# Kernel tuning notes

Hardware: AMD Instinct MI355X
Metric: run time of the kernel (lower is better)

Reference implementation:

```python
import jax, jax.numpy as jnp
import numpy as np

N = 100000          # nodes
E = 3200000         # edges (avg degree 32)
F_IN = 128
HID = [128, 256, 128, 64, 32]
EPS = 1e-5


def setup_inputs() -> dict:
    key = jax.random.key(0)
    ks = jax.random.split(key, 64)
    inp = {}
    inp["x"] = jax.random.normal(ks[0], (N, F_IN), dtype=jnp.float32)
    inp["edge_index"] = jax.random.randint(ks[1], (2, E), 0, N, dtype=jnp.int64)
    dims = [F_IN] + HID
    k = 2
    for i in range(len(HID)):
        fan_in = dims[i]
        inp[f"W{i}"] = jax.random.normal(ks[k], (dims[i], dims[i + 1]), dtype=jnp.float32) / np.sqrt(fan_in); k += 1
        inp[f"b{i}"] = jnp.zeros((dims[i + 1],), dtype=jnp.float32)
        inp[f"g{i}"] = jnp.ones((dims[i + 1],), dtype=jnp.float32)
        inp[f"be{i}"] = jnp.zeros((dims[i + 1],), dtype=jnp.float32)
    inp["fc_w"] = jax.random.normal(ks[k], (HID[-1], 1), dtype=jnp.float32) / np.sqrt(HID[-1])
    inp["fc_b"] = jnp.zeros((1,), dtype=jnp.float32)
    return inp


def _gcn_forward(x, edge_index, Ws, bs, gs, bes, fc_w, fc_b):
    src, dst = edge_index[0], edge_index[1]
    # symmetric-normalized adjacency with self-loops (PyG GCNConv default,
    # edge_weight=None -> all-ones). deg = in-degree + 1 (self-loop).
    deg = jax.ops.segment_sum(jnp.ones((E,), x.dtype), dst, num_segments=N) + 1.0
    dis = jax.lax.rsqrt(deg)                 # deg^{-1/2}
    di = 1.0 / deg                           # self-loop norm deg^{-1}
    norm = (dis[src] * dis[dst])[:, None]    # [E,1]
    for W, b, g, be in zip(Ws, bs, gs, bes):
        h = x @ W                                                        # [N,d']
        x = jax.ops.segment_sum(norm * h[src], dst, num_segments=N)
        x = x + di[:, None] * h + b                                      # conv out
        mu = jnp.mean(x, axis=0)
        var = jnp.mean(jnp.square(x - mu), axis=0)
        x = (x - mu) * jax.lax.rsqrt(var + EPS) * g + be                 # BatchNorm1d
        x = jax.nn.relu(x)                                               # dropout = eval identity
    edge_emb = x[src] * x[dst]                                           # [E, 32]
    return jax.nn.sigmoid(edge_emb @ fc_w + fc_b)                        # [E, 1]


def reference(x, edge_index, W0, b0, g0, be0, W1, b1, g1, be1, W2, b2, g2, be2,
              W3, b3, g3, be3, W4, b4, g4, be4, fc_w, fc_b):
    Ws = [W0, W1, W2, W3, W4]
    bs = [b0, b1, b2, b3, b4]
    gs = [g0, g1, g2, g3, g4]
    bes = [be0, be1, be2, be3, be4]
    return _gcn_forward(x, edge_index, Ws, bs, gs, bes, fc_w, fc_b)
```

## Files before the change

kernel.cpp:

```cpp
#include <hip/hip_runtime.h>
#include <hip/hip_fp16.h>
#include <cstddef>

#define NN 100000
#define EE 3200000
#define EPSB 1e-5f
#define NB 391
#define BCAP 10240
#define BNBLK 512

typedef _Float16 half8 __attribute__((ext_vector_type(8)));
typedef float floatx4 __attribute__((ext_vector_type(4)));


__global__ __launch_bounds__(256) void k_bscat(const int* __restrict__ src,
                                               const int* __restrict__ dst,
                                               int* __restrict__ bcur,
                                               unsigned* __restrict__ barr) {
    __shared__ int hist[NB];
    __shared__ int base[NB];
    int tid = threadIdx.x;
    for (int b = tid; b < NB; b += 256) hist[b] = 0;
    __syncthreads();
    int e0 = blockIdx.x * 4096;
    int d[16], s[16];
    #pragma unroll
    for (int j = 0; j < 16; j++) {
        int e = e0 + j * 256 + tid;
        if (e < EE) {
            d[j] = dst[e];
            s[j] = src[e];
            atomicAdd(&hist[d[j] >> 8], 1);
        } else d[j] = -1;
    }
    __syncthreads();
    for (int b = tid; b < NB; b += 256) {
        int c = hist[b];
        base[b] = (c > 0) ? atomicAdd(&bcur[b], c) : 0;
        hist[b] = 0;
    }
    __syncthreads();
    #pragma unroll
    for (int j = 0; j < 16; j++) {
        if (d[j] >= 0) {
            int b = d[j] >> 8;
            int r = atomicAdd(&hist[b], 1);
            barr[(size_t)b * BCAP + base[b] + r] =
                (unsigned)s[j] | ((unsigned)(d[j] & 255) << 17);
        }
    }
}

__global__ __launch_bounds__(1024) void k_bdeg(const int* __restrict__ bcur,
                                               const unsigned* __restrict__ barr,
                                               int* __restrict__ degcnt,
                                               float* __restrict__ dis) {
    __shared__ int h[256];
    int b = blockIdx.x;
    if (threadIdx.x < 256) h[threadIdx.x] = 0;
    __syncthreads();
    int cnt = bcur[b];
    const unsigned* p = barr + (size_t)b * BCAP;
    for (int t = threadIdx.x; t < cnt; t += 1024)
        atomicAdd(&h[(p[t] >> 17) & 255], 1);
    __syncthreads();
    if (threadIdx.x < 256) {
        int node = (b << 8) + threadIdx.x;
        if (node < NN) {
            int dg = h[threadIdx.x];
            degcnt[node] = dg;
            dis[node] = rsqrtf((float)dg + 1.0f);
        }
    }
}

__global__ __launch_bounds__(1024) void k_place(const int* __restrict__ bcur,
                                                const unsigned* __restrict__ barr,
                                                const int* __restrict__ rowptr,
                                                int* __restrict__ col) {
    __shared__ int cur[256];
    int b = blockIdx.x;
    if (threadIdx.x < 256) {
        int node = (b << 8) + threadIdx.x;
        cur[threadIdx.x] = (node < NN) ? rowptr[node] : 0;
    }
    __syncthreads();
    int cnt = bcur[b];
    const unsigned* p = barr + (size_t)b * BCAP;
    for (int t = threadIdx.x; t < cnt; t += 1024) {
        unsigned e = p[t];
        int pos = atomicAdd(&cur[(e >> 17) & 255], 1);
        col[pos] = (int)(e & 0x1FFFFu);
    }
}

__global__ void k_scan_block(const int* __restrict__ in, int* __restrict__ out,
                             int* __restrict__ blksum, int n) {
    __shared__ int s[1024];
    int i = blockIdx.x * 1024 + threadIdx.x;
    int v = (i < n) ? in[i] : 0;
    s[threadIdx.x] = v;
    __syncthreads();
    for (int off = 1; off < 1024; off <<= 1) {
        int t = (threadIdx.x >= off) ? s[threadIdx.x - off] : 0;
        __syncthreads();
        s[threadIdx.x] += t;
        __syncthreads();
    }
    if (i < n) out[i] = s[threadIdx.x] - v;
    if (threadIdx.x == 1023) blksum[blockIdx.x] = s[1023];
}

__global__ void k_scan_top(int* __restrict__ blksum, int nb) {
    if (threadIdx.x == 0) {
        int acc = 0;
        for (int b = 0; b < nb; b++) { int v = blksum[b]; blksum[b] = acc; acc += v; }
    }
}

__global__ void k_scan_add(int* __restrict__ out, const int* __restrict__ blksum, int n) {
    int i = blockIdx.x * 1024 + threadIdx.x;
    if (i < n) out[i] += blksum[blockIdx.x];
}


__global__ void k_f2h(const float4* __restrict__ in, uint2* __restrict__ out, int n4) {
    int t = blockIdx.x * blockDim.x + threadIdx.x;
    if (t >= n4) return;
    float4 v = in[t];
    union { __half2 h; unsigned u; } a, b;
    a.h = __floats2half2_rn(v.x, v.y);
    b.h = __floats2half2_rn(v.z, v.w);
    out[t] = make_uint2(a.u, b.u);
}

__global__ void k_wpack_all(const float* __restrict__ W0, const float* __restrict__ W1,
                            const float* __restrict__ W2, const float* __restrict__ W3,
                            const float* __restrict__ W4, __half* __restrict__ Wp) {
    const int offs[6] = {0, 16384, 49152, 81920, 90112, 92160};
    const int Ks[5] = {128, 128, 256, 128, 64};
    const int Ns[5] = {128, 256, 128, 64, 32};
    const float* Ws[5] = {W0, W1, W2, W3, W4};
    int t = blockIdx.x * blockDim.x + threadIdx.x;
    if (t >= 92160) return;
    int l = 0;
    while (t >= offs[l + 1]) l++;
    int local = t - offs[l];
    int N = Ns[l], K = Ks[l];
    int k = local / N, n = local - k * N;
    Wp[(size_t)offs[l] + (size_t)n * K + k] = __float2half(Ws[l][local]);
}


template<int NT, bool OUT16, bool ABN>
__global__ __launch_bounds__(256) void k_mgemm(const void* __restrict__ Av,
                                               const __half* __restrict__ Wp,
                                               void* __restrict__ Cv,
                                               int M, int K, int N,
                                               const float* __restrict__ dis,
                                               const float* __restrict__ bias,
                                               const float* __restrict__ AB) {
    constexpr int TN = NT * 16;
    __shared__ __half Ash[128][40];
    __shared__ __half Bsh[TN][40];
    int tid  = threadIdx.x;
    int wave = tid >> 6;
    int lane = tid & 63;
    int quad = lane >> 4;
    int l16  = lane & 15;
    int bm = blockIdx.x * 128;
    int bn = blockIdx.y * TN;

    floatx4 acc[2][NT];
    #pragma unroll
    for (int mt = 0; mt < 2; mt++)
        #pragma unroll
        for (int nt = 0; nt < NT; nt++)
            acc[mt][nt] = (floatx4){0.f, 0.f, 0.f, 0.f};

    for (int k0 = 0; k0 < K; k0 += 32) {
        #pragma unroll
        for (int it = 0; it < 2; it++) {
            int u = tid + it * 256;
            int row = u >> 2, seg = u & 3;
            int grow = bm + row;
            if (ABN) {
                const float* Af = (const float*)Av;
                int f0 = k0 + seg * 8;
                uint4 o = make_uint4(0, 0, 0, 0);
                if (grow < M) {
                    float4 x0 = *(const float4*)&Af[(size_t)grow * K + f0];
                    float4 x1 = *(const float4*)&Af[(size_t)grow * K + f0 + 4];
                    float4 a0 = *(const float4*)&AB[f0];
                    float4 a1 = *(const float4*)&AB[f0 + 4];
                    float4 c0 = *(const float4*)&AB[K + f0];
                    float4 c1 = *(const float4*)&AB[K + f0 + 4];
                    float h0 = fmaxf(x0.x * a0.x + c0.x, 0.f);
                    float h1 = fmaxf(x0.y * a0.y + c0.y, 0.f);
                    float h2 = fmaxf(x0.z * a0.z + c0.z, 0.f);
                    float h3 = fmaxf(x0.w * a0.w + c0.w, 0.f);
                    float h4 = fmaxf(x1.x * a1.x + c1.x, 0.f);
                    float h5 = fmaxf(x1.y * a1.y + c1.y, 0.f);
                    float h6 = fmaxf(x1.z * a1.z + c1.z, 0.f);
                    float h7 = fmaxf(x1.w * a1.w + c1.w, 0.f);
                    union { __half2 h; unsigned u; } p0, p1, p2, p3;
                    p0.h = __floats2half2_rn(h0, h1);
                    p1.h = __floats2half2_rn(h2, h3);
                    p2.h = __floats2half2_rn(h4, h5);
                    p3.h = __floats2half2_rn(h6, h7);
                    o = make_uint4(p0.u, p1.u, p2.u, p3.u);
                }
                *(uint4*)&Ash[row][seg * 8] = o;
            } else {
                const __half* A = (const __half*)Av;
                uint4 v = make_uint4(0, 0, 0, 0);
                if (grow < M) v = *(const uint4*)&A[(size_t)grow * K + k0 + seg * 8];
                *(uint4*)&Ash[row][seg * 8] = v;
            }
        }
        if (tid < TN * 4) {
            int n = tid >> 2, seg = tid & 3;
            uint4 v = *(const uint4*)&Wp[(size_t)(bn + n) * K + k0 + seg * 8];
            *(uint4*)&Bsh[n][seg * 8] = v;
        }
        __syncthreads();
        half8 a[2], b[NT];
        #pragma unroll
        for (int mt = 0; mt < 2; mt++)
            a[mt] = *(const half8*)&Ash[wave * 32 + mt * 16 + l16][quad * 8];
        #pragma unroll
        for (int nt = 0; nt < NT; nt++)
            b[nt] = *(const half8*)&Bsh[nt * 16 + l16][quad * 8];
        #pragma unroll
        for (int mt = 0; mt < 2; mt++)
            #pragma unroll
            for (int nt = 0; nt < NT; nt++)
                acc[mt][nt] = __builtin_amdgcn_mfma_f32_16x16x32_f16(
                    a[mt], b[nt], acc[mt][nt], 0, 0, 0);
        __syncthreads();
    }

    #pragma unroll
    for (int mt = 0; mt < 2; mt++) {
        #pragma unroll
        for (int r = 0; r < 4; r++) {
            int grow = bm + wave * 32 + mt * 16 + quad * 4 + r;
            if (grow >= M) continue;
            if (OUT16) {
                float ds = dis[grow];
                __half* C = (__half*)Cv;
                #pragma unroll
                for (int nt = 0; nt < NT; nt++) {
                    int gcol = bn + nt * 16 + l16;
                    C[(size_t)grow * N + gcol] = __float2half(ds * acc[mt][nt][r]);
                }
            } else {
                float* C = (float*)Cv;
                #pragma unroll
                for (int nt = 0; nt < NT; nt++) {
                    int gcol = bn + nt * 16 + l16;
                    C[(size_t)grow * N + gcol] = acc[mt][nt][r] + bias[gcol];
                }
            }
        }
    }
}


__global__ __launch_bounds__(256) void k_q8p8(const uint4* __restrict__ H,
                                              uint2* __restrict__ q8,
                                              float* __restrict__ scq, int total) {
    int t = blockIdx.x * 256 + threadIdx.x;
    if (t >= total) return;
    uint4 v = H[t];
    const __half2* hp = (const __half2*)&v;
    float h[8];
    #pragma unroll
    for (int k = 0; k < 4; k++) {
        float2 f = __half22float2(hp[k]);
        h[2 * k] = f.x; h[2 * k + 1] = f.y;
    }
    float m = fabsf(h[0]);
    #pragma unroll
    for (int k = 1; k < 8; k++) m = fmaxf(m, fabsf(h[k]));
    float inv = m > 0.f ? 127.f / m : 0.f;
    unsigned b[8];
    #pragma unroll
    for (int k = 0; k < 8; k++) {
        float f = fminf(fmaxf(h[k] * inv, -127.f), 127.f);
        b[k] = (unsigned)(f + 128.5f);
    }
    q8[t] = make_uint2(b[0] | (b[1] << 8) | (b[2] << 16) | (b[3] << 24),
                       b[4] | (b[5] << 8) | (b[6] << 16) | (b[7] << 24));
    scq[t] = m * (1.f / 127.f);
}

__global__ void k_nscale_q8(const float* __restrict__ X, const float* __restrict__ AB,
                            const float* __restrict__ dis, uint2* __restrict__ q8,
                            float* __restrict__ scq) {
    int t = blockIdx.x * blockDim.x + threadIdx.x;
    if (t >= NN * 16) return;
    int row = t >> 4;
    int f0 = (t & 15) * 8;
    float ds = dis[row];
    float4 x0 = *(const float4*)&X[(size_t)row * 128 + f0];
    float4 x1 = *(const float4*)&X[(size_t)row * 128 + f0 + 4];
    float4 a0 = *(const float4*)&AB[f0];
    float4 a1 = *(const float4*)&AB[f0 + 4];
    float4 c0 = *(const float4*)&AB[128 + f0];
    float4 c1 = *(const float4*)&AB[128 + f0 + 4];
    float h[8];
    h[0] = ds * fmaxf(x0.x * a0.x + c0.x, 0.f);
    h[1] = ds * fmaxf(x0.y * a0.y + c0.y, 0.f);
    h[2] = ds * fmaxf(x0.z * a0.z + c0.z, 0.f);
    h[3] = ds * fmaxf(x0.w * a0.w + c0.w, 0.f);
    h[4] = ds * fmaxf(x1.x * a1.x + c1.x, 0.f);
    h[5] = ds * fmaxf(x1.y * a1.y + c1.y, 0.f);
    h[6] = ds * fmaxf(x1.z * a1.z + c1.z, 0.f);
    h[7] = ds * fmaxf(x1.w * a1.w + c1.w, 0.f);
    float m = h[0];
    #pragma unroll
    for (int k = 1; k < 8; k++) m = fmaxf(m, h[k]);
    m = fmaxf(m, __shfl_xor(m, 1));
    float inv = m > 0.f ? 255.f / m : 0.f;
    unsigned b[8];
    #pragma unroll
    for (int k = 0; k < 8; k++)
        b[k] = (unsigned)(fminf(h[k] * inv, 255.f) + 0.5f);
    q8[t] = make_uint2(b[0] | (b[1] << 8) | (b[2] << 16) | (b[3] << 24),
                       b[4] | (b[5] << 8) | (b[6] << 16) | (b[7] << 24));
    if ((t & 1) == 0) scq[t >> 1] = m * (1.f / 255.f);
}


__device__ __forceinline__ void acc_q8s2(float* acc, const uint4& r,
                                         const float2& s, float& c0, float& c1) {
    const unsigned* w = (const unsigned*)&r;
    c0 += s.x; c1 += s.y;
    #pragma unroll
    for (int q = 0; q < 4; q++) {
        unsigned v = w[q];
        float sq = (q < 2) ? s.x : s.y;
        acc[4 * q + 0] = fmaf(sq, (float)(v & 0xffu), acc[4 * q + 0]);
        acc[4 * q + 1] = fmaf(sq, (float)((v >> 8) & 0xffu), acc[4 * q + 1]);
        acc[4 * q + 2] = fmaf(sq, (float)((v >> 16) & 0xffu), acc[4 * q + 2]);
        acc[4 * q + 3] = fmaf(sq, (float)(v >> 24), acc[4 * q + 3]);
    }
}

template<int TPN>
__global__ __launch_bounds__(256) void k_agg_q8s(const uint4* __restrict__ Q,
                                                 const float* __restrict__ sc,
                                                 float* __restrict__ outf,
                                                 const int* __restrict__ rowptr,
                                                 const int* __restrict__ degcnt,
                                                 const int* __restrict__ colv,
                                                 const float* __restrict__ dis,
                                                 const float* __restrict__ bias) {
    constexpr int G = 256 / TPN;
    int g    = threadIdx.x / TPN;
    int lane = threadIdx.x % TPN;
    int i = blockIdx.x * G + g;
    if (i >= NN) return;
    int beg = rowptr[i];
    int cnt = degcnt[i];
    const uint4*  base = Q + lane;
    const float2* scb  = (const float2*)sc + lane;
    float acc[16] = {};
    float c0 = 0.f, c1 = 0.f;
    int e = 0;
    for (; e + 8 <= cnt; e += 8) {
        int c[8];
        #pragma unroll
        for (int j = 0; j < 8; j++) c[j] = colv[beg + e + j];
        uint4 r[8];
        float2 s[8];
        #pragma unroll
        for (int j = 0; j < 8; j++) {
            r[j] = base[(size_t)c[j] * TPN];
            s[j] = scb[(size_t)c[j] * TPN];
        }
        #pragma unroll
        for (int j = 0; j < 8; j++) acc_q8s2(acc, r[j], s[j], c0, c1);
    }
    for (; e < cnt; e++) {
        int c = colv[beg + e];
        uint4 r = base[(size_t)c * TPN];
        acc_q8s2(acc, r, scb[(size_t)c * TPN], c0, c1);
    }
    uint4 rs = base[(size_t)i * TPN];
    acc_q8s2(acc, rs, scb[(size_t)i * TPN], c0, c1);
    float ds = dis[i];
    float zp0 = 128.f * c0, zp1 = 128.f * c1;
    float o[16];
    #pragma unroll
    for (int k = 0; k < 16; k++) o[k] = ds * (acc[k] - (k < 8 ? zp0 : zp1));
    float4* out = (float4*)outf;
    const float4* bi = (const float4*)bias;
    size_t ob = (size_t)i * (4 * TPN) + lane * 4;
    #pragma unroll
    for (int j = 0; j < 4; j++) {
        float4 b = bi[lane * 4 + j];
        out[ob + j] = make_float4(o[4 * j] + b.x, o[4 * j + 1] + b.y,
                                  o[4 * j + 2] + b.z, o[4 * j + 3] + b.w);
    }
}

__device__ __forceinline__ void acc_q8u(float* acc, const uint4& r, float s) {
    const unsigned* w = (const unsigned*)&r;
    #pragma unroll
    for (int q = 0; q < 4; q++) {
        unsigned v = w[q];
        acc[4 * q + 0] = fmaf(s, (float)(v & 0xffu), acc[4 * q + 0]);
        acc[4 * q + 1] = fmaf(s, (float)((v >> 8) & 0xffu), acc[4 * q + 1]);
        acc[4 * q + 2] = fmaf(s, (float)((v >> 16) & 0xffu), acc[4 * q + 2]);
        acc[4 * q + 3] = fmaf(s, (float)(v >> 24), acc[4 * q + 3]);
    }
}

template<int TPN>
__global__ __launch_bounds__(256) void k_agg_q8u(const uint4* __restrict__ Q,
                                                 const float* __restrict__ sc,
                                                 __half* __restrict__ out16,
                                                 const int* __restrict__ rowptr,
                                                 const int* __restrict__ degcnt,
                                                 const int* __restrict__ colv,
                                                 const float* __restrict__ dis) {
    constexpr int G = 256 / TPN;
    int g    = threadIdx.x / TPN;
    int lane = threadIdx.x % TPN;
    int i = blockIdx.x * G + g;
    if (i >= NN) return;
    int beg = rowptr[i];
    int cnt = degcnt[i];
    const uint4* base = Q + lane;
    const float* scb  = sc + lane;
    float acc[16] = {};
    int e = 0;
    for (; e + 8 <= cnt; e += 8) {
        int c[8];
        #pragma unroll
        for (int j = 0; j < 8; j++) c[j] = colv[beg + e + j];
        uint4 r[8];
        float s[8];
        #pragma unroll
        for (int j = 0; j < 8; j++) {
            r[j] = base[(size_t)c[j] * TPN];
            s[j] = scb[(size_t)c[j] * TPN];
        }
        #pragma unroll
        for (int j = 0; j < 8; j++) acc_q8u(acc, r[j], s[j]);
    }
    for (; e < cnt; e++) {
        int c = colv[beg + e];
        uint4 r = base[(size_t)c * TPN];
        acc_q8u(acc, r, scb[(size_t)c * TPN]);
    }
    uint4 rs = base[(size_t)i * TPN];
    acc_q8u(acc, rs, scb[(size_t)i * TPN]);
    float ds = dis[i];
    float o[16];
    #pragma unroll
    for (int k = 0; k < 16; k++) o[k] = ds * acc[k];
    uint4 ov0, ov1;
    __half2* p0 = (__half2*)&ov0;
    __half2* p1 = (__half2*)&ov1;
    #pragma unroll
    for (int k = 0; k < 4; k++) {
        p0[k] = __floats2half2_rn(o[2 * k], o[2 * k + 1]);
        p1[k] = __floats2half2_rn(o[8 + 2 * k], o[9 + 2 * k]);
    }
    uint4* out = (uint4*)out16;
    size_t ob = (size_t)i * (2 * TPN) + lane * 2;
    out[ob]     = ov0;
    out[ob + 1] = ov1;
}

__device__ __forceinline__ void acc_row(float* acc, const uint4& r) {
    const __half2* hp = (const __half2*)&r;
    #pragma unroll
    for (int k = 0; k < 4; k++) {
        float2 f2 = __half22float2(hp[k]);
        acc[2 * k]     += f2.x;
        acc[2 * k + 1] += f2.y;
    }
}

template<int TPN, bool OUT16>
__global__ __launch_bounds__(256) void k_agg_h(const uint4* __restrict__ Hs,
                                               void* __restrict__ outv,
                                               const int* __restrict__ rowptr,
                                               const int* __restrict__ degcnt,
                                               const int* __restrict__ colv,
                                               const float* __restrict__ dis,
                                               const float* __restrict__ bias) {
    constexpr int G = 256 / TPN;
    int g    = threadIdx.x / TPN;
    int lane = threadIdx.x % TPN;
    int i = blockIdx.x * G + g;
    if (i >= NN) return;
    int beg = rowptr[i];
    int cnt = degcnt[i];
    const uint4* base = Hs + lane;
    float acc[8] = {};
    int e = 0;
    for (; e + 16 <= cnt; e += 16) {
        int c[16];
        #pragma unroll
        for (int j = 0; j < 16; j++) c[j] = colv[beg + e + j];
        uint4 r[16];
        #pragma unroll
        for (int j = 0; j < 16; j++) r[j] = base[(size_t)c[j] * TPN];
        #pragma unroll
        for (int j = 0; j < 16; j++) acc_row(acc, r[j]);
    }
    for (; e + 4 <= cnt; e += 4) {
        int c[4];
        #pragma unroll
        for (int j = 0; j < 4; j++) c[j] = colv[beg + e + j];
        uint4 r[4];
        #pragma unroll
        for (int j = 0; j < 4; j++) r[j] = base[(size_t)c[j] * TPN];
        #pragma unroll
        for (int j = 0; j < 4; j++) acc_row(acc, r[j]);
    }
    for (; e < cnt; e++) {
        uint4 r = base[(size_t)colv[beg + e] * TPN];
        acc_row(acc, r);
    }
    uint4 rs = base[(size_t)i * TPN];
    acc_row(acc, rs);
    float ds = dis[i];
    float o[8];
    #pragma unroll
    for (int k = 0; k < 8; k++) o[k] = ds * acc[k];
    if (OUT16) {
        uint4 ov;
        __half2* op = (__half2*)&ov;
        #pragma unroll
        for (int k = 0; k < 4; k++) op[k] = __floats2half2_rn(o[2 * k], o[2 * k + 1]);
        ((uint4*)outv)[(size_t)i * TPN + lane] = ov;
    } else {
        float4 b0 = ((const float4*)bias)[lane * 2];
        float4 b1 = ((const float4*)bias)[lane * 2 + 1];
        o[0] += b0.x; o[1] += b0.y; o[2] += b0.z; o[3] += b0.w;
        o[4] += b1.x; o[5] += b1.y; o[6] += b1.z; o[7] += b1.w;
        float4* out = (float4*)outv;
        size_t ob = (size_t)i * (2 * TPN) + lane * 2;
        out[ob]     = make_float4(o[0], o[1], o[2], o[3]);
        out[ob + 1] = make_float4(o[4], o[5], o[6], o[7]);
    }
}


template<int D>
__global__ __launch_bounds__(256) void k_bnpart(const float4* __restrict__ X4,
                                                float* __restrict__ partial) {
    constexpr int Q   = D / 4;
    constexpr int RPI = 256 / Q;
    int tq = threadIdx.x % Q;
    int rg = threadIdx.x / Q;
    int chunk = (NN + BNBLK - 1) / BNBLK;
    int r0 = blockIdx.x * chunk;
    int r1 = r0 + chunk; if (r1 > NN) r1 = NN;
    float4 s  = {0.f, 0.f, 0.f, 0.f};
    float4 s2 = {0.f, 0.f, 0.f, 0.f};
    for (int r = r0 + rg; r < r1; r += RPI) {
        float4 v = X4[(size_t)r * Q + tq];
        s.x += v.x; s.y += v.y; s.z += v.z; s.w += v.w;
        s2.x += v.x * v.x; s2.y += v.y * v.y; s2.z += v.z * v.z; s2.w += v.w * v.w;
    }
    __shared__ float4 ls[256], ls2[256];
    ls[threadIdx.x] = s; ls2[threadIdx.x] = s2;
    __syncthreads();
    if (threadIdx.x < Q) {
        float4 a = ls[threadIdx.x], b = ls2[threadIdx.x];
        #pragma unroll
        for (int g = 1; g < RPI; g++) {
            float4 u = ls[g * Q + threadIdx.x], w = ls2[g * Q + threadIdx.x];
            a.x += u.x; a.y += u.y; a.z += u.z; a.w += u.w;
            b.x += w.x; b.y += w.y; b.z += w.z; b.w += w.w;
        }
        *(float4*)&partial[(size_t)blockIdx.x * 2 * D + threadIdx.x * 4]     = a;
        *(float4*)&partial[(size_t)blockIdx.x * 2 * D + D + threadIdx.x * 4] = b;
    }
}

template<int D>
__global__ __launch_bounds__(1024) void k_bnfin2(const float* __restrict__ partial,
                                                 const float* __restrict__ g,
                                                 const float* __restrict__ be,
                                                 float* __restrict__ AB) {
    constexpr int G = 1024 / D;
    int f  = threadIdx.x % D;
    int gr = threadIdx.x / D;
    float sum = 0.f, sq = 0.f;
    for (int b = gr; b < BNBLK; b += G) {
        sum += partial[(size_t)b * 2 * D + f];
        sq  += partial[(size_t)b * 2 * D + D + f];
    }
    __shared__ float ls[1024], ls2[1024];
    ls[threadIdx.x] = sum; ls2[threadIdx.x] = sq;
    __syncthreads();
    if (threadIdx.x < D) {
        float a = ls[threadIdx.x], b = ls2[threadIdx.x];
        for (int k = 1; k < G; k++) {
            a += ls[k * D + threadIdx.x];
            b += ls2[k * D + threadIdx.x];
        }
        float mu  = a / (float)NN;
        float var = b / (float)NN - mu * mu;
        var = fmaxf(var, 0.f);
        float inv = rsqrtf(var + EPSB);
        float sc = g[threadIdx.x] * inv;
        AB[threadIdx.x]     = sc;
        AB[D + threadIdx.x] = be[threadIdx.x] - mu * sc;
    }
}

__global__ void k_norm16(const float4* __restrict__ X, const float* __restrict__ AB,
                         uint2* __restrict__ Y, int d, int total4) {
    int t = blockIdx.x * blockDim.x + threadIdx.x;
    if (t >= total4) return;
    int f0 = (t * 4) & (d - 1);
    float4 v = X[t];
    float a0 = AB[f0],     a1 = AB[f0 + 1], a2 = AB[f0 + 2], a3 = AB[f0 + 3];
    float c0 = AB[d + f0], c1 = AB[d + f0 + 1], c2 = AB[d + f0 + 2], c3 = AB[d + f0 + 3];
    float o0 = fmaxf(v.x * a0 + c0, 0.f);
    float o1 = fmaxf(v.y * a1 + c1, 0.f);
    float o2 = fmaxf(v.z * a2 + c2, 0.f);
    float o3 = fmaxf(v.w * a3 + c3, 0.f);
    union { __half2 h; unsigned u; } p, q;
    p.h = __floats2half2_rn(o0, o1);
    q.h = __floats2half2_rn(o2, o3);
    Y[t] = make_uint2(p.u, q.u);
}


__global__ __launch_bounds__(256) void k_edge16(const uint4* __restrict__ X,
                                                const int* __restrict__ src,
                                                const int* __restrict__ dst,
                                                const float* __restrict__ fcw,
                                                const float* __restrict__ fcb,
                                                float* __restrict__ out) {
    int lane = threadIdx.x & 3;
    size_t t = (size_t)blockIdx.x * 256 + threadIdx.x;
    int eid = (int)(t >> 2);
    if (eid >= EE) return;
    int s = src[eid], d = dst[eid];
    uint4 av = X[(size_t)s * 4 + lane];
    uint4 bv = X[(size_t)d * 4 + lane];
    const __half2* ap = (const __half2*)&av;
    const __half2* bp2 = (const __half2*)&bv;
    float v = 0.f;
    #pragma unroll
    for (int k = 0; k < 4; k++) {
        float2 fa = __half22float2(ap[k]);
        float2 fb = __half22float2(bp2[k]);
        float w0 = fcw[lane * 8 + 2 * k];
        float w1 = fcw[lane * 8 + 2 * k + 1];
        v += fa.x * fb.x * w0 + fa.y * fb.y * w1;
    }
    v += __shfl_xor(v, 1, 4);
    v += __shfl_xor(v, 2, 4);
    if (lane == 0) out[eid] = 1.f / (1.f + expf(-(v + fcb[0])));
}


extern "C" void kernel_launch(void* const* d_in, const int* in_sizes, int n_in,
                              void* d_out, int out_size, void* d_ws, size_t ws_size,
                              hipStream_t stream) {
    const float* x0 = (const float*)d_in[0];
    const int* ei   = (const int*)d_in[1];
    const int* srcv = ei;
    const int* dstv = ei + EE;
    const float *W[5], *bp[5], *gp[5], *bep[5];
    int idx = 2;
    for (int l = 0; l < 5; l++) {
        W[l]   = (const float*)d_in[idx++];
        bp[l]  = (const float*)d_in[idx++];
        gp[l]  = (const float*)d_in[idx++];
        bep[l] = (const float*)d_in[idx++];
    }
    const float* fcw = (const float*)d_in[22];
    const float* fcb = (const float*)d_in[23];

    char* ws = (char*)d_ws;
    size_t off = 0;
    auto alloc = [&](size_t bytes) -> void* {
        void* p = ws + off;
        off = (off + bytes + 255) & ~(size_t)255;
        return p;
    };
    float*    bufA    = (float*)   alloc((size_t)NN * 256 * 4);
    __half*   act16   = (__half*)  alloc((size_t)NN * 256 * 2);
    __half*   x16     = (__half*)  alloc((size_t)NN * 128 * 2);
    __half*   Hh      = (__half*)  alloc((size_t)NN * 128 * 2);
    unsigned* barr    = (unsigned*)alloc((size_t)NB * BCAP * 4);
    int*      colv    = (int*)     alloc((size_t)EE * 4);
    int*      rowptr  = (int*)     alloc((size_t)NN * 4);
    int*      degcnt  = (int*)     alloc((size_t)NN * 4);
    float*    dis     = (float*)   alloc((size_t)NN * 4);
    int*      bcur    = (int*)     alloc((size_t)NB * 4);
    int*      scnblk  = (int*)     alloc(4096);
    float*    bnpart  = (float*)   alloc((size_t)BNBLK * 512 * 4);
    float*    bnAB    = (float*)   alloc(512 * 4);
    __half*   Wp      = (__half*)  alloc((size_t)92160 * 2);
    float*    scq     = (float*)   alloc((size_t)NN * 16 * 4);
    const int woff[5] = {0, 16384, 49152, 81920, 90112};

    unsigned char* q8 = (unsigned char*)barr;

    hipMemsetAsync(bcur, 0, (size_t)NB * 4, stream);
    k_bscat<<<(EE + 4095) / 4096, 256, 0, stream>>>(srcv, dstv, bcur, barr);
    k_bdeg<<<NB, 1024, 0, stream>>>(bcur, barr, degcnt, dis);
    int nScanBlk = (NN + 1023) / 1024;
    k_scan_block<<<nScanBlk, 1024, 0, stream>>>(degcnt, rowptr, scnblk, NN);
    k_scan_top<<<1, 64, 0, stream>>>(scnblk, nScanBlk);
    k_scan_add<<<nScanBlk, 1024, 0, stream>>>(rowptr, scnblk, NN);
    k_place<<<NB, 1024, 0, stream>>>(bcur, barr, rowptr, colv);

    k_f2h<<<(NN * 128 / 4 + 255) / 256, 256, 0, stream>>>(
        (const float4*)x0, (uint2*)x16, NN * 128 / 4);
    k_wpack_all<<<(92160 + 255) / 256, 256, 0, stream>>>(W[0], W[1], W[2], W[3], W[4], Wp);

    int gx = (NN + 127) / 128;

    {
        dim3 grid(gx, 128 / 64);
        k_mgemm<4, true, false><<<grid, 256, 0, stream>>>(x16, Wp + woff[0], Hh, NN, 128, 128, dis, nullptr, nullptr);
        k_q8p8<<<NN * 16 / 256, 256, 0, stream>>>((const uint4*)Hh, (uint2*)q8, scq, NN * 16);
        k_agg_q8s<8><<<(NN + 31) / 32, 256, 0, stream>>>(
            (const uint4*)q8, scq, bufA, rowptr, degcnt, colv, dis, bp[0]);
        k_bnpart<128><<<BNBLK, 256, 0, stream>>>((const float4*)bufA, bnpart);
        k_bnfin2<128><<<1, 1024, 0, stream>>>(bnpart, gp[0], bep[0], bnAB);
        k_nscale_q8<<<(NN * 16 + 255) / 256, 256, 0, stream>>>(bufA, bnAB, dis, (uint2*)q8, scq);
    }
    {
        k_agg_q8u<8><<<(NN + 31) / 32, 256, 0, stream>>>(
            (const uint4*)q8, scq, act16, rowptr, degcnt, colv, dis);
        dim3 grid(gx, 256 / 64);
        k_mgemm<4, false, false><<<grid, 256, 0, stream>>>(act16, Wp + woff[1], bufA, NN, 128, 256, nullptr, bp[1], nullptr);
        k_bnpart<256><<<BNBLK, 256, 0, stream>>>((const float4*)bufA, bnpart);
        k_bnfin2<256><<<1, 1024, 0, stream>>>(bnpart, gp[1], bep[1], bnAB);
    }
    {
        dim3 grid(gx, 128 / 64);
        k_mgemm<4, true, true><<<grid, 256, 0, stream>>>(bufA, Wp + woff[2], Hh, NN, 256, 128, dis, nullptr, bnAB);
        k_agg_h<16, false><<<(NN + 15) / 16, 256, 0, stream>>>(
            (const uint4*)Hh, bufA, rowptr, degcnt, colv, dis, bp[2]);
        k_bnpart<128><<<BNBLK, 256, 0, stream>>>((const float4*)bufA, bnpart);
        k_bnfin2<128><<<1, 1024, 0, stream>>>(bnpart, gp[2], bep[2], bnAB);
    }
    {
        dim3 grid(gx, 64 / 64);
        k_mgemm<4, true, true><<<grid, 256, 0, stream>>>(bufA, Wp + woff[3], Hh, NN, 128, 64, dis, nullptr, bnAB);
        k_agg_h<8, false><<<(NN + 31) / 32, 256, 0, stream>>>(
            (const uint4*)Hh, bufA, rowptr, degcnt, colv, dis, bp[3]);
        k_bnpart<64><<<BNBLK, 256, 0, stream>>>((const float4*)bufA, bnpart);
        k_bnfin2<64><<<1, 1024, 0, stream>>>(bnpart, gp[3], bep[3], bnAB);
    }
    {
        dim3 grid(gx, 1);
        k_mgemm<2, true, true><<<grid, 256, 0, stream>>>(bufA, Wp + woff[4], Hh, NN, 64, 32, dis, nullptr, bnAB);
        k_agg_h<4, false><<<(NN + 63) / 64, 256, 0, stream>>>(
            (const uint4*)Hh, bufA, rowptr, degcnt, colv, dis, bp[4]);
        k_bnpart<32><<<BNBLK, 256, 0, stream>>>((const float4*)bufA, bnpart);
        k_bnfin2<32><<<1, 1024, 0, stream>>>(bnpart, gp[4], bep[4], bnAB);
        int total4 = NN * 32 / 4;
        k_norm16<<<(total4 + 255) / 256, 256, 0, stream>>>(
            (const float4*)bufA, bnAB, (uint2*)act16, 32, total4);
    }

    size_t edgeThreads = (size_t)EE * 4;
    k_edge16<<<(unsigned)((edgeThreads + 255) / 256), 256, 0, stream>>>(
        (const uint4*)act16, srcv, dstv, fcw, fcb, (float*)d_out);
}
```

Before: 984.5 us.

## Interleave int8 rows with fp16 scales in one 160-byte record

```diff
diff --git a/kernel.cpp b/kernel.cpp
--- a/kernel.cpp
+++ b/kernel.cpp
@@ -267,11 +267,12 @@
 }
 
 
-__global__ __launch_bounds__(256) void k_q8p8(const uint4* __restrict__ H,
-                                              uint2* __restrict__ q8,
-                                              float* __restrict__ scq, int total) {
+__global__ __launch_bounds__(256) void k_q8i(const uint4* __restrict__ H,
+                                             unsigned* __restrict__ q8d,
+                                             int total) {
     int t = blockIdx.x * 256 + threadIdx.x;
     if (t >= total) return;
+    int row = t >> 4, sub = t & 15;
     uint4 v = H[t];
     const __half2* hp = (const __half2*)&v;
     float h[8];
@@ -290,18 +291,20 @@
         float f = fminf(fmaxf(h[k] * inv, -127.f), 127.f);
         b[k] = (unsigned)(f + 128.5f);
     }
-    q8[t] = make_uint2(b[0] | (b[1] << 8) | (b[2] << 16) | (b[3] << 24),
-                       b[4] | (b[5] << 8) | (b[6] << 16) | (b[7] << 24));
-    scq[t] = m * (1.f / 127.f);
-}
-
-__global__ void k_nscale_q8(const float* __restrict__ X, const float* __restrict__ AB,
-                            const float* __restrict__ dis, uint2* __restrict__ q8,
-                            float* __restrict__ scq) {
+    int db = row * 40 + sub * 2;
+    q8d[db]     = b[0] | (b[1] << 8) | (b[2] << 16) | (b[3] << 24);
+    q8d[db + 1] = b[4] | (b[5] << 8) | (b[6] << 16) | (b[7] << 24);
+    ((__half*)q8d)[row * 80 + 64 + sub] = __float2half(m * (1.f / 127.f));
+}
+
+__global__ void k_nscale_q8i(const float* __restrict__ X, const float* __restrict__ AB,
+                             const float* __restrict__ dis,
+                             unsigned* __restrict__ q8d) {
     int t = blockIdx.x * blockDim.x + threadIdx.x;
     if (t >= NN * 16) return;
     int row = t >> 4;
-    int f0 = (t & 15) * 8;
+    int sub = t & 15;
+    int f0 = sub * 8;
     float ds = dis[row];
     float4 x0 = *(const float4*)&X[(size_t)row * 128 + f0];
     float4 x1 = *(const float4*)&X[(size_t)row * 128 + f0 + 4];
@@ -321,15 +324,15 @@
     float m = h[0];
     #pragma unroll
     for (int k = 1; k < 8; k++) m = fmaxf(m, h[k]);
-    m = fmaxf(m, __shfl_xor(m, 1));
     float inv = m > 0.f ? 255.f / m : 0.f;
     unsigned b[8];
     #pragma unroll
     for (int k = 0; k < 8; k++)
         b[k] = (unsigned)(fminf(h[k] * inv, 255.f) + 0.5f);
-    q8[t] = make_uint2(b[0] | (b[1] << 8) | (b[2] << 16) | (b[3] << 24),
-                       b[4] | (b[5] << 8) | (b[6] << 16) | (b[7] << 24));
-    if ((t & 1) == 0) scq[t >> 1] = m * (1.f / 255.f);
+    int db = row * 40 + sub * 2;
+    q8d[db]     = b[0] | (b[1] << 8) | (b[2] << 16) | (b[3] << 24);
+    q8d[db + 1] = b[4] | (b[5] << 8) | (b[6] << 16) | (b[7] << 24);
+    ((__half*)q8d)[row * 80 + 64 + sub] = __float2half(m * (1.f / 255.f));
 }
 
 
@@ -348,24 +351,39 @@
     }
 }
 
-template<int TPN>
+__device__ __forceinline__ void acc_q8u2(float* acc, const uint4& r, const float2& s) {
+    const unsigned* w = (const unsigned*)&r;
+    #pragma unroll
+    for (int q = 0; q < 4; q++) {
+        unsigned v = w[q];
+        float sq = (q < 2) ? s.x : s.y;
+        acc[4 * q + 0] = fmaf(sq, (float)(v & 0xffu), acc[4 * q + 0]);
+        acc[4 * q + 1] = fmaf(sq, (float)((v >> 8) & 0xffu), acc[4 * q + 1]);
+        acc[4 * q + 2] = fmaf(sq, (float)((v >> 16) & 0xffu), acc[4 * q + 2]);
+        acc[4 * q + 3] = fmaf(sq, (float)(v >> 24), acc[4 * q + 3]);
+    }
+}
+
+__device__ __forceinline__ float2 h2f(unsigned u) {
+    union { unsigned u; __half2 h; } c; c.u = u;
+    return __half22float2(c.h);
+}
+
 __global__ __launch_bounds__(256) void k_agg_q8s(const uint4* __restrict__ Q,
-                                                 const float* __restrict__ sc,
                                                  float* __restrict__ outf,
                                                  const int* __restrict__ rowptr,
                                                  const int* __restrict__ degcnt,
                                                  const int* __restrict__ colv,
                                                  const float* __restrict__ dis,
                                                  const float* __restrict__ bias) {
-    constexpr int G = 256 / TPN;
-    int g    = threadIdx.x / TPN;
-    int lane = threadIdx.x % TPN;
-    int i = blockIdx.x * G + g;
+    int g    = threadIdx.x >> 3;
+    int lane = threadIdx.x & 7;
+    int i = blockIdx.x * 32 + g;
     if (i >= NN) return;
     int beg = rowptr[i];
     int cnt = degcnt[i];
-    const uint4*  base = Q + lane;
-    const float2* scb  = (const float2*)sc + lane;
+    const uint4*    base = Q + lane;
+    const unsigned* scd  = (const unsigned*)Q;
     float acc[16] = {};
     float c0 = 0.f, c1 = 0.f;
     int e = 0;
@@ -374,22 +392,22 @@
         #pragma unroll
         for (int j = 0; j < 8; j++) c[j] = colv[beg + e + j];
         uint4 r[8];
-        float2 s[8];
+        unsigned u[8];
         #pragma unroll
         for (int j = 0; j < 8; j++) {
-            r[j] = base[(size_t)c[j] * TPN];
-            s[j] = scb[(size_t)c[j] * TPN];
-        }
-        #pragma unroll
-        for (int j = 0; j < 8; j++) acc_q8s2(acc, r[j], s[j], c0, c1);
+            r[j] = base[(size_t)c[j] * 10];
+            u[j] = scd[(size_t)c[j] * 40 + 32 + lane];
+        }
+        #pragma unroll
+        for (int j = 0; j < 8; j++) acc_q8s2(acc, r[j], h2f(u[j]), c0, c1);
     }
     for (; e < cnt; e++) {
         int c = colv[beg + e];
-        uint4 r = base[(size_t)c * TPN];
-        acc_q8s2(acc, r, scb[(size_t)c * TPN], c0, c1);
-    }
-    uint4 rs = base[(size_t)i * TPN];
-    acc_q8s2(acc, rs, scb[(size_t)i * TPN], c0, c1);
+        uint4 r = base[(size_t)c * 10];
+        acc_q8s2(acc, r, h2f(scd[(size_t)c * 40 + 32 + lane]), c0, c1);
+    }
+    uint4 rs = base[(size_t)i * 10];
+    acc_q8s2(acc, rs, h2f(scd[(size_t)i * 40 + 32 + lane]), c0, c1);
     float ds = dis[i];
     float zp0 = 128.f * c0, zp1 = 128.f * c1;
     float o[16];
@@ -397,7 +415,7 @@
     for (int k = 0; k < 16; k++) o[k] = ds * (acc[k] - (k < 8 ? zp0 : zp1));
     float4* out = (float4*)outf;
     const float4* bi = (const float4*)bias;
-    size_t ob = (size_t)i * (4 * TPN) + lane * 4;
+    size_t ob = (size_t)i * 32 + lane * 4;
     #pragma unroll
     for (int j = 0; j < 4; j++) {
         float4 b = bi[lane * 4 + j];
@@ -406,35 +424,20 @@
     }
 }
 
-__device__ __forceinline__ void acc_q8u(float* acc, const uint4& r, float s) {
-    const unsigned* w = (const unsigned*)&r;
-    #pragma unroll
-    for (int q = 0; q < 4; q++) {
-        unsigned v = w[q];
-        acc[4 * q + 0] = fmaf(s, (float)(v & 0xffu), acc[4 * q + 0]);
-        acc[4 * q + 1] = fmaf(s, (float)((v >> 8) & 0xffu), acc[4 * q + 1]);
-        acc[4 * q + 2] = fmaf(s, (float)((v >> 16) & 0xffu), acc[4 * q + 2]);
-        acc[4 * q + 3] = fmaf(s, (float)(v >> 24), acc[4 * q + 3]);
-    }
-}
-
-template<int TPN>
 __global__ __launch_bounds__(256) void k_agg_q8u(const uint4* __restrict__ Q,
-                                                 const float* __restrict__ sc,
                                                  __half* __restrict__ out16,
                                                  const int* __restrict__ rowptr,
                                                  const int* __restrict__ degcnt,
                                                  const int* __restrict__ colv,
                                                  const float* __restrict__ dis) {
-    constexpr int G = 256 / TPN;
-    int g    = threadIdx.x / TPN;
-    int lane = threadIdx.x % TPN;
-    int i = blockIdx.x * G + g;
+    int g    = threadIdx.x >> 3;
+    int lane = threadIdx.x & 7;
+    int i = blockIdx.x * 32 + g;
     if (i >= NN) return;
     int beg = rowptr[i];
     int cnt = degcnt[i];
-    const uint4* base = Q + lane;
-    const float* scb  = sc + lane;
+    const uint4*    base = Q + lane;
+    const unsigned* scd  = (const unsigned*)Q;
     float acc[16] = {};
     int e = 0;
     for (; e + 8 <= cnt; e += 8) {
@@ -442,22 +445,22 @@
         #pragma unroll
         for (int j = 0; j < 8; j++) c[j] = colv[beg + e + j];
         uint4 r[8];
-        float s[8];
+        unsigned u[8];
         #pragma unroll
         for (int j = 0; j < 8; j++) {
-            r[j] = base[(size_t)c[j] * TPN];
-            s[j] = scb[(size_t)c[j] * TPN];
-        }
-        #pragma unroll
-        for (int j = 0; j < 8; j++) acc_q8u(acc, r[j], s[j]);
+            r[j] = base[(size_t)c[j] * 10];
+            u[j] = scd[(size_t)c[j] * 40 + 32 + lane];
+        }
+        #pragma unroll
+        for (int j = 0; j < 8; j++) acc_q8u2(acc, r[j], h2f(u[j]));
     }
     for (; e < cnt; e++) {
         int c = colv[beg + e];
-        uint4 r = base[(size_t)c * TPN];
-        acc_q8u(acc, r, scb[(size_t)c * TPN]);
-    }
-    uint4 rs = base[(size_t)i * TPN];
-    acc_q8u(acc, rs, scb[(size_t)i * TPN]);
+        uint4 r = base[(size_t)c * 10];
+        acc_q8u2(acc, r, h2f(scd[(size_t)c * 40 + 32 + lane]));
+    }
+    uint4 rs = base[(size_t)i * 10];
+    acc_q8u2(acc, rs, h2f(scd[(size_t)i * 40 + 32 + lane]));
     float ds = dis[i];
     float o[16];
     #pragma unroll
@@ -471,7 +474,7 @@
         p1[k] = __floats2half2_rn(o[8 + 2 * k], o[9 + 2 * k]);
     }
     uint4* out = (uint4*)out16;
-    size_t ob = (size_t)i * (2 * TPN) + lane * 2;
+    size_t ob = (size_t)i * 16 + lane * 2;
     out[ob]     = ov0;
     out[ob + 1] = ov1;
 }
@@ -504,25 +507,15 @@
     const uint4* base = Hs + lane;
     float acc[8] = {};
     int e = 0;
-    for (; e + 16 <= cnt; e += 16) {
-        int c[16];
-        #pragma unroll
-        for (int j = 0; j < 16; j++) c[j] = colv[beg + e + j];
-        uint4 r[16];
-        #pragma unroll
-        for (int j = 0; j < 16; j++) r[j] = base[(size_t)c[j] * TPN];
-        #pragma unroll
-        for (int j = 0; j < 16; j++) acc_row(acc, r[j]);
-    }
-    for (; e + 4 <= cnt; e += 4) {
-        int c[4];
-        #pragma unroll
-        for (int j = 0; j < 4; j++) c[j] = colv[beg + e + j];
-        uint4 r[4];
-        #pragma unroll
-        for (int j = 0; j < 4; j++) r[j] = base[(size_t)c[j] * TPN];
-        #pragma unroll
-        for (int j = 0; j < 4; j++) acc_row(acc, r[j]);
+    for (; e + 8 <= cnt; e += 8) {
+        int c[8];
+        #pragma unroll
+        for (int j = 0; j < 8; j++) c[j] = colv[beg + e + j];
+        uint4 r[8];
+        #pragma unroll
+        for (int j = 0; j < 8; j++) r[j] = base[(size_t)c[j] * TPN];
+        #pragma unroll
+        for (int j = 0; j < 8; j++) acc_row(acc, r[j]);
     }
     for (; e < cnt; e++) {
         uint4 r = base[(size_t)colv[beg + e] * TPN];
@@ -706,10 +699,9 @@
     float*    bnpart  = (float*)   alloc((size_t)BNBLK * 512 * 4);
     float*    bnAB    = (float*)   alloc(512 * 4);
     __half*   Wp      = (__half*)  alloc((size_t)92160 * 2);
-    float*    scq     = (float*)   alloc((size_t)NN * 16 * 4);
     const int woff[5] = {0, 16384, 49152, 81920, 90112};
 
-    unsigned char* q8 = (unsigned char*)barr;
+    unsigned* q8 = (unsigned*)barr;
 
     hipMemsetAsync(bcur, 0, (size_t)NB * 4, stream);
     k_bscat<<<(EE + 4095) / 4096, 256, 0, stream>>>(srcv, dstv, bcur, barr);
@@ -729,16 +721,16 @@
     {
         dim3 grid(gx, 128 / 64);
         k_mgemm<4, true, false><<<grid, 256, 0, stream>>>(x16, Wp + woff[0], Hh, NN, 128, 128, dis, nullptr, nullptr);
-        k_q8p8<<<NN * 16 / 256, 256, 0, stream>>>((const uint4*)Hh, (uint2*)q8, scq, NN * 16);
-        k_agg_q8s<8><<<(NN + 31) / 32, 256, 0, stream>>>(
-            (const uint4*)q8, scq, bufA, rowptr, degcnt, colv, dis, bp[0]);
+        k_q8i<<<NN * 16 / 256, 256, 0, stream>>>((const uint4*)Hh, q8, NN * 16);
+        k_agg_q8s<<<(NN + 31) / 32, 256, 0, stream>>>(
+            (const uint4*)q8, bufA, rowptr, degcnt, colv, dis, bp[0]);
         k_bnpart<128><<<BNBLK, 256, 0, stream>>>((const float4*)bufA, bnpart);
         k_bnfin2<128><<<1, 1024, 0, stream>>>(bnpart, gp[0], bep[0], bnAB);
-        k_nscale_q8<<<(NN * 16 + 255) / 256, 256, 0, stream>>>(bufA, bnAB, dis, (uint2*)q8, scq);
+        k_nscale_q8i<<<(NN * 16 + 255) / 256, 256, 0, stream>>>(bufA, bnAB, dis, q8);
     }
     {
-        k_agg_q8u<8><<<(NN + 31) / 32, 256, 0, stream>>>(
-            (const uint4*)q8, scq, act16, rowptr, degcnt, colv, dis);
+        k_agg_q8u<<<(NN + 31) / 32, 256, 0, stream>>>(
+            (const uint4*)q8, act16, rowptr, degcnt, colv, dis);
         dim3 grid(gx, 256 / 64);
         k_mgemm<4, false, false><<<grid, 256, 0, stream>>>(act16, Wp + woff[1], bufA, NN, 128, 256, nullptr, bp[1], nullptr);
         k_bnpart<256><<<BNBLK, 256, 0, stream>>>((const float4*)bufA, bnpart);
```

Measured after the change: 997.9 us. Within noise of the previous version (+1.4%).
